# Optimization experiments

Measured on AMD Instinct MI355X. Metric: run time of the kernel, lower is better.

## Reference

```python
import jax, jax.numpy as jnp
import numpy as np

B, CIN, H, W = 16, 256, 48, 48
K, CD, MULTI = 64, 64, 1
GAMMA = (1.0 - 1e-10) ** (1.0 ** 0.6)  # iter = 1


def _ln(v, s, b, eps=1e-5):
    m = v.mean(-1, keepdims=True)
    var = ((v - m) ** 2).mean(-1, keepdims=True)
    return (v - m) / jnp.sqrt(var + eps) * s + b


def _spatial_masks():
    # pairwise squared distance between (i,j) grid coords, N = H*W
    ii, jj = jnp.meshgrid(jnp.arange(H, dtype=jnp.float32), jnp.arange(W, dtype=jnp.float32), indexing='ij')
    coord = jnp.stack([ii.ravel(), jj.ravel()], axis=1)  # [N,2]
    sq = (coord ** 2).sum(-1, keepdims=True)             # [N,1]
    d2 = sq - 2.0 * (coord @ coord.T) + sq.T             # [N,N]
    m = jnp.exp(-jnp.sqrt(jnp.abs(d2)))
    A = m / m.sum(0, keepdims=True)  # column-normalized (torch sums dim=1 of [B,N,N])
    cur, out = A, []
    for _ in range(MULTI):
        cur = cur @ A  # A^(num+2)
        out.append(cur)
    return out


def setup_inputs() -> dict:
    key = jax.random.key(0)
    ks = jax.random.split(key, 3)
    x = jax.random.normal(ks[0], (B, CIN, H, W), jnp.float32)
    clusters = jax.random.normal(ks[1], (1, K, CD), jnp.float32) * 0.1
    pi = jnp.ones((1, K), jnp.float32) / K
    cov = jnp.ones((1, K), jnp.float32)
    w_proj = jax.random.normal(ks[2], (CD, CIN), jnp.float32) / np.sqrt(CIN)
    nt_scale = jnp.ones((CD,), jnp.float32)
    nt_bias = jnp.zeros((CD,), jnp.float32)
    pn_scale = jnp.ones((K * MULTI,), jnp.float32)
    pn_bias = jnp.zeros((K * MULTI,), jnp.float32)
    return dict(x=x, clusters=clusters, pi=pi, cov=cov, w_proj=w_proj,
                nt_scale=nt_scale, nt_bias=nt_bias, pn_scale=pn_scale, pn_bias=pn_bias)


def reference(x, clusters, pi, cov, w_proj, nt_scale, nt_bias, pn_scale, pn_bias):
    N = H * W
    # 1x1 conv projection -> tokens [B,N,CD]
    xf = jnp.einsum('bihw,ci->bhwc', x, w_proj).reshape(B, N, CD)
    # normalized templates (batch-invariant)
    t = _ln(clusters[0], nt_scale, nt_bias)  # [K,CD]
    # squared euclidean distance via expansion (avoids [B,CD,N,K] intermediate)
    x2 = (xf ** 2).sum(-1)  # [B,N]
    t2 = (t ** 2).sum(-1)   # [K]
    d = x2[:, :, None] + t2[None, None, :] - 2.0 * jnp.einsum('bnc,kc->bnk', xf, t)
    logits = jnp.log(pi[0] / jnp.sqrt(cov[0])) - d / cov[0] / 2.0
    attn = jax.nn.softmax(logits, axis=-1)  # [B,N,K]
    # EM-style updates
    pi_new = pi + GAMMA * (attn.sum(1) / N - pi)                     # [B,K]
    attn_n = attn + 1e-8
    attn_n = attn_n / attn_n.sum(-2, keepdims=True)                  # normalize over N
    t_new = clusters + GAMMA * (jnp.einsum('bnc,bnk->bkc', xf, attn_n) - clusters)  # [B,K,CD]
    tn2 = (t_new ** 2).sum(-1)  # [B,K]
    d2 = x2[:, :, None] + tn2[:, None, :] - 2.0 * jnp.einsum('bnc,bkc->bnk', xf, t_new)
    cov_new = cov + GAMMA * ((d2 * attn_n).sum(1) - cov)             # [B,K]
    # spatial distance-encoding masks (stop-gradient / constant w.r.t. params)
    masks = _spatial_masks()
    outp = jnp.concatenate([jnp.einsum('bnk,nm->bkm', attn_n, M) for M in masks], axis=1)  # [B,K*MULTI,N]
    outp = _ln(outp.transpose(0, 2, 1), pn_scale, pn_bias).transpose(0, 2, 1)
    outp = outp.reshape(B, K * MULTI, H, W)
    attn_out = attn.transpose(0, 2, 1).reshape(B, K, H, W)
    return outp, attn_out, t_new, pi_new, cov_new
```

## Files before the change

### kernel.cpp

```cpp
#include <hip/hip_runtime.h>
#include <hip/hip_bf16.h>
#include <math.h>

#define B_   16
#define CIN_ 256
#define H_   48
#define W_   48
#define N_   2304
#define K_   64
#define CD_  64

#define GAMMA_F 0.9999999999f
#define LUT_N  4419

using f32x4  = __attribute__((ext_vector_type(4))) float;
using bf16x8 = __attribute__((ext_vector_type(8))) short;
using s16x4  = __attribute__((ext_vector_type(4))) short;

__device__ __forceinline__ void split_bf(float x, short& hi, short& lo) {
  unsigned u = __builtin_bit_cast(unsigned, x);
  unsigned r = (u + 0x7FFFu + ((u >> 16) & 1u)) & 0xFFFF0000u;
  hi = (short)(r >> 16);
  float res = x - __builtin_bit_cast(float, r);
  unsigned u2 = __builtin_bit_cast(unsigned, res);
  unsigned r2 = u2 + 0x7FFFu + ((u2 >> 16) & 1u);
  lo = (short)(r2 >> 16);
}

constexpr size_t OFF_XF    = 0;
constexpr size_t OFF_ANT   = OFF_XF    + (size_t)B_*N_*CD_;
constexpr size_t OFF_T     = OFF_ANT   + (size_t)B_*K_*N_;
constexpr size_t OFF_T2    = OFF_T     + (size_t)K_*CD_;
constexpr size_t OFF_LOGPI = OFF_T2    + K_;
constexpr size_t OFF_I2C   = OFF_LOGPI + K_;
constexpr size_t OFF_X2    = OFF_I2C   + K_;
constexpr size_t OFF_CS    = OFF_X2    + (size_t)B_*N_;
constexpr size_t OFF_ICN   = OFF_CS    + (size_t)B_*K_;
constexpr size_t OFF_MASKH = OFF_ICN   + (size_t)B_*K_;
constexpr size_t OFF_MASKL = OFF_MASKH + (size_t)N_*N_/2;

constexpr size_t OUT_OUTP = 0;
constexpr size_t OUT_ATTN = (size_t)B_*K_*N_;
constexpr size_t OUT_TNEW = OUT_ATTN + (size_t)B_*K_*N_;
constexpr size_t OUT_PI   = OUT_TNEW + (size_t)B_*K_*CD_;
constexpr size_t OUT_COV  = OUT_PI   + (size_t)B_*K_;

__global__ __launch_bounds__(256) void k_proj(const float* __restrict__ x, const float* __restrict__ wp,
                                              float* __restrict__ xf) {
  __shared__ float xs[32][64];
  __shared__ float ws_[32][65];
  int b = blockIdx.y, n0 = blockIdx.x * 64;
  int tid = threadIdx.x;
  int nn = tid & 63, cg = tid >> 6;
  float acc[16];
#pragma unroll
  for (int j = 0; j < 16; j++) acc[j] = 0.f;
  for (int i0 = 0; i0 < CIN_; i0 += 32) {
#pragma unroll
    for (int j = 0; j < 8; j++) {
      int ii = cg * 8 + j;
      xs[ii][nn] = x[((size_t)b * CIN_ + i0 + ii) * N_ + n0 + nn];
    }
    {
      int c = tid >> 2, iq = (tid & 3) * 8;
#pragma unroll
      for (int j = 0; j < 8; j++)
        ws_[iq + j][c] = wp[(size_t)c * CIN_ + i0 + iq + j];
    }
    __syncthreads();
#pragma unroll
    for (int ii = 0; ii < 32; ++ii) {
      float xv = xs[ii][nn];
#pragma unroll
      for (int j = 0; j < 16; j++) acc[j] += xv * ws_[ii][cg * 16 + j];
    }
    __syncthreads();
  }
  float* dst = xf + ((size_t)b * N_ + n0 + nn) * CD_ + cg * 16;
#pragma unroll
  for (int j4 = 0; j4 < 4; j4++)
    *(float4*)(dst + j4 * 4) = make_float4(acc[j4*4], acc[j4*4+1], acc[j4*4+2], acc[j4*4+3]);
}

__global__ void k_templ(const float* __restrict__ clusters, const float* __restrict__ pi,
                        const float* __restrict__ cov, const float* __restrict__ nsc,
                        const float* __restrict__ nbi, float* __restrict__ t, float* __restrict__ t2,
                        float* __restrict__ logpi, float* __restrict__ i2c) {
  int k = threadIdx.x;
  float v[CD_];
  float m = 0;
#pragma unroll
  for (int c = 0; c < CD_; c++) { v[c] = clusters[k * CD_ + c]; m += v[c]; }
  m /= CD_;
  float var = 0;
#pragma unroll
  for (int c = 0; c < CD_; c++) { float d = v[c] - m; var += d * d; }
  var /= CD_;
  float inv = 1.f / sqrtf(var + 1e-5f);
  float s2 = 0;
#pragma unroll
  for (int c = 0; c < CD_; c++) {
    float tv = (v[c] - m) * inv * nsc[c] + nbi[c];
    t[k * CD_ + c] = tv;
    s2 += tv * tv;
  }
  t2[k] = s2;
  float p = pi[k], cv = cov[k];
  logpi[k] = logf(p) - 0.5f * logf(cv);
  i2c[k] = 0.5f / cv;
}

__global__ __launch_bounds__(256) void k_attn(const float* __restrict__ xf, const float* __restrict__ t,
                                              const float* __restrict__ t2, const float* __restrict__ logpi,
                                              const float* __restrict__ i2c, float* __restrict__ ant,
                                              float* __restrict__ aout, float* __restrict__ x2o) {
  __shared__ __align__(16) float ts[K_ * CD_];
  __shared__ float t2s[K_], lps[K_], ics[K_];
  int tid = threadIdx.x;
  for (int i = tid; i < K_ * CD_; i += 256) ts[i] = t[i];
  if (tid < K_) { t2s[tid] = t2[tid]; lps[tid] = logpi[tid]; ics[tid] = i2c[tid]; }
  __syncthreads();
  int b = blockIdx.y;
  int n = blockIdx.x * 256 + tid;
  const float4* xr = (const float4*)(xf + ((size_t)b * N_ + n) * CD_);
  float4 xv[16];
#pragma unroll
  for (int i = 0; i < 16; i++) xv[i] = xr[i];
  float x2 = 0;
#pragma unroll
  for (int i = 0; i < 16; i++) x2 += xv[i].x * xv[i].x + xv[i].y * xv[i].y + xv[i].z * xv[i].z + xv[i].w * xv[i].w;
  x2o[(size_t)b * N_ + n] = x2;
  float lg[K_];
#pragma unroll
  for (int k = 0; k < K_; k++) {
    const float4* tk = (const float4*)(ts + k * CD_);
    float dot = 0;
#pragma unroll
    for (int i = 0; i < 16; i++) {
      float4 tv = tk[i];
      dot += xv[i].x * tv.x + xv[i].y * tv.y + xv[i].z * tv.z + xv[i].w * tv.w;
    }
    lg[k] = lps[k] - (x2 + t2s[k] - 2.f * dot) * ics[k];
  }
  float mx = lg[0];
#pragma unroll
  for (int k = 1; k < K_; k++) mx = fmaxf(mx, lg[k]);
  float sum = 0;
#pragma unroll
  for (int k = 0; k < K_; k++) { lg[k] = __expf(lg[k] - mx); sum += lg[k]; }
  float inv = 1.f / sum;
  size_t base = (size_t)b * K_ * N_ + n;
#pragma unroll
  for (int k = 0; k < K_; k++) {
    float v = lg[k] * inv;
    ant[base + (size_t)k * N_] = v;
    aout[base + (size_t)k * N_] = v;
  }
}

__global__ __launch_bounds__(256) void k_colsum2(const float* __restrict__ ant, float* __restrict__ colsum) {
  int r = blockIdx.x, tid = threadIdx.x;
  const float* row = ant + (size_t)r * N_;
  float s = 0;
  for (int n = tid; n < N_; n += 256) s += row[n];
#pragma unroll
  for (int off = 32; off; off >>= 1) s += __shfl_down(s, off);
  __shared__ float red[4];
  if ((tid & 63) == 0) red[tid >> 6] = s;
  __syncthreads();
  if (tid == 0) colsum[r] = red[0] + red[1] + red[2] + red[3];
}

__global__ void k_pinew(const float* __restrict__ colsum, const float* __restrict__ pi,
                        float* __restrict__ pi_out, float* __restrict__ icn) {
  int b = blockIdx.x, k = threadIdx.x;
  float cs = colsum[b * K_ + k];
  float p = pi[k];
  pi_out[b * K_ + k] = p + GAMMA_F * (cs / (float)N_ - p);
  icn[b * K_ + k] = 1.f / (cs + (float)N_ * 1e-8f);
}

__global__ __launch_bounds__(256) void k_tnew_cov(const float* __restrict__ ant, const float* __restrict__ icn,
                                                  const float* __restrict__ xf, const float* __restrict__ x2,
                                                  const float* __restrict__ clusters, const float* __restrict__ cov,
                                                  float* __restrict__ tnew_out, float* __restrict__ cov_out) {
  int k = blockIdx.x, b = blockIdx.y;
  int tid = threadIdx.x;
  int c = tid & 63, g = tid >> 6;
  const float* arow = ant + ((size_t)b * K_ + k) * N_;
  const float* x2r = x2 + (size_t)b * N_;
  float acc = 0, ax2 = 0;
#pragma unroll 4
  for (int n = g; n < N_; n += 4) {
    float a = arow[n] + 1e-8f;
    acc += a * xf[((size_t)b * N_ + n) * CD_ + c];
    ax2 += a * x2r[n];
  }
  __shared__ float red[4][64];
  __shared__ float red2[4];
  red[g][c] = acc;
  if (c == 0) red2[g] = ax2;
  __syncthreads();
  if (tid < 64) {
    float icnv = icn[b * K_ + k];
    float s = (red[0][c] + red[1][c] + red[2][c] + red[3][c]) * icnv;
    float cl = clusters[k * CD_ + c];
    float tv = cl + GAMMA_F * (s - cl);
    tnew_out[((size_t)b * K_ + k) * CD_ + c] = tv;
    float sq = tv * tv;
    float st = s * tv;
#pragma unroll
    for (int off = 32; off; off >>= 1) { sq += __shfl_down(sq, off); st += __shfl_down(st, off); }
    if (c == 0) {
      float ax2t = (red2[0] + red2[1] + red2[2] + red2[3]) * icnv;
      float cv = cov[k];
      float csum = ax2t + sq - 2.f * st;
      cov_out[b * K_ + k] = cv + GAMMA_F * (csum - cv);
    }
  }
}

__global__ __launch_bounds__(256) void k_amean(const float* __restrict__ ant, const float* __restrict__ icn,
                                               float* __restrict__ amean) {
  int b = blockIdx.y;
  int n = blockIdx.x * 256 + threadIdx.x;
  const float* base = ant + (size_t)b * K_ * N_ + n;
  const float* ic = icn + b * K_;
  float s = 0;
#pragma unroll 8
  for (int k = 0; k < K_; k++)
    s += (base[(size_t)k * N_] + 1e-8f) * ic[k];
  amean[(size_t)b * N_ + n] = s * (1.f / (float)K_);
}

__global__ __launch_bounds__(256) void k_mask(short* __restrict__ MH, short* __restrict__ ML) {
  __shared__ float lut[LUT_N];
  __shared__ float red[4];
  const int m = blockIdx.x;
  const int mi = m / W_, mj = m % W_;
  const int tid = threadIdx.x;
  for (int i = tid; i < LUT_N; i += 256) lut[i] = __expf(-sqrtf((float)i));
  __syncthreads();
  float e[N_ / 256];
  float s = 0;
#pragma unroll
  for (int it = 0; it < N_ / 256; it++) {
    int n = it * 256 + tid;
    int ni = n / W_, nj = n - (n / W_) * W_;
    int dx = ni - mi, dy = nj - mj;
    e[it] = lut[dx * dx + dy * dy];
    s += e[it];
  }
#pragma unroll
  for (int off = 32; off; off >>= 1) s += __shfl_down(s, off);
  if ((tid & 63) == 0) red[tid >> 6] = s;
  __syncthreads();
  const float imc = 1.f / (red[0] + red[1] + red[2] + red[3]);
#pragma unroll
  for (int it = 0; it < N_ / 256; it++) {
    int n = it * 256 + tid;
    short h, l;
    split_bf(e[it] * imc, h, l);
    MH[(size_t)m * N_ + n] = h;
    ML[(size_t)m * N_ + n] = l;
  }
}


__global__ __launch_bounds__(256) void gemm1_mfma(const float* __restrict__ Am, const float* __restrict__ icn,
                                                  const float* __restrict__ amean,
                                                  const short* __restrict__ MaskH, const short* __restrict__ MaskL,
                                                  short* __restrict__ YdH, short* __restrict__ YdL) {
  __shared__ __align__(16) short Ah[64][40];
  __shared__ __align__(16) short Al[64][40];
  __shared__ __align__(16) short Bh[64][40];
  __shared__ __align__(16) short Bl[64][40];
  const int tid = threadIdx.x;
  const int b = blockIdx.y;
  const int m0 = b * 64, n0 = blockIdx.x * 64;
  const int lane = tid & 63, w = tid >> 6;
  const int fr = lane & 15, quad = lane >> 4;
  const int srow = tid >> 2;
  const int skq  = (tid & 3) * 8;
  const float ic = icn[m0 + srow];
  const float badd = 1e-8f * ic;
  const size_t mrow = (size_t)(n0 + srow) * N_;
  f32x4 acc[4] = {};
  for (int k0 = 0; k0 < N_; k0 += 32) {
    const float* ap = Am + (size_t)(m0 + srow) * N_ + k0 + skq;
    const float* mp = amean + (size_t)b * N_ + k0 + skq;
    float va[8];
    {
      float4 a0 = *(const float4*)ap;
      float4 a1 = *(const float4*)(ap + 4);
      float4 u0 = *(const float4*)mp;
      float4 u1 = *(const float4*)(mp + 4);
      va[0] = fmaf(a0.x, ic, badd) - u0.x; va[1] = fmaf(a0.y, ic, badd) - u0.y;
      va[2] = fmaf(a0.z, ic, badd) - u0.z; va[3] = fmaf(a0.w, ic, badd) - u0.w;
      va[4] = fmaf(a1.x, ic, badd) - u1.x; va[5] = fmaf(a1.y, ic, badd) - u1.y;
      va[6] = fmaf(a1.z, ic, badd) - u1.z; va[7] = fmaf(a1.w, ic, badd) - u1.w;
    }
    bf16x8 avh, avl;
#pragma unroll
    for (int j = 0; j < 8; j++) { short h, l; split_bf(va[j], h, l); avh[j] = h; avl[j] = l; }
    *(bf16x8*)&Ah[srow][skq] = avh;
    *(bf16x8*)&Al[srow][skq] = avl;
    *(bf16x8*)&Bh[srow][skq] = *(const bf16x8*)&MaskH[mrow + k0 + skq];
    *(bf16x8*)&Bl[srow][skq] = *(const bf16x8*)&MaskL[mrow + k0 + skq];
    __syncthreads();
    bf16x8 afh = *(const bf16x8*)&Ah[w * 16 + fr][quad * 8];
    bf16x8 afl = *(const bf16x8*)&Al[w * 16 + fr][quad * 8];
#pragma unroll
    for (int ns = 0; ns < 4; ns++) {
      bf16x8 bfh = *(const bf16x8*)&Bh[ns * 16 + fr][quad * 8];
      bf16x8 bfl = *(const bf16x8*)&Bl[ns * 16 + fr][quad * 8];
      acc[ns] = __builtin_amdgcn_mfma_f32_16x16x32_bf16(afh, bfh, acc[ns], 0, 0, 0);
      acc[ns] = __builtin_amdgcn_mfma_f32_16x16x32_bf16(afh, bfl, acc[ns], 0, 0, 0);
      acc[ns] = __builtin_amdgcn_mfma_f32_16x16x32_bf16(afl, bfh, acc[ns], 0, 0, 0);
    }
    __syncthreads();
  }
  const size_t rbase = (size_t)(m0 + w * 16 + fr) * N_ + n0;
#pragma unroll
  for (int ns = 0; ns < 4; ns++) {
    s16x4 h4, l4;
#pragma unroll
    for (int reg = 0; reg < 4; reg++) { short h, l; split_bf(acc[ns][reg], h, l); h4[reg] = h; l4[reg] = l; }
    *(s16x4*)&YdH[rbase + ns * 16 + quad * 4] = h4;
    *(s16x4*)&YdL[rbase + ns * 16 + quad * 4] = l4;
  }
}

__global__ __launch_bounds__(256) void gemm2_ln_mfma(const short* __restrict__ YdH, const short* __restrict__ YdL,
                                                     const short* __restrict__ MaskH, const short* __restrict__ MaskL,
                                                     const float* __restrict__ pns, const float* __restrict__ pnb,
                                                     float* __restrict__ outp) {
  __shared__ __align__(16) short Ah[64][40];
  __shared__ __align__(16) short Al[64][40];
  __shared__ __align__(16) short Bh[64][40];
  __shared__ __align__(16) short Bl[64][40];
  __shared__ __align__(16) float S[64][68];
  __shared__ float rstd[64], sc[64], bi[64];
  const int tid = threadIdx.x;
  const int b = blockIdx.y;
  const int m0 = b * 64, n0 = blockIdx.x * 64;
  const int lane = tid & 63, w = tid >> 6;
  const int fr = lane & 15, quad = lane >> 4;
  const int srow = tid >> 2;
  const int skq  = (tid & 3) * 8;
  const size_t mrow = (size_t)(n0 + srow) * N_;
  if (tid < 64) { sc[tid] = pns[tid]; bi[tid] = pnb[tid]; }
  f32x4 acc[4] = {};
  for (int k0 = 0; k0 < N_; k0 += 32) {
    const size_t aoff = (size_t)(m0 + srow) * N_ + k0 + skq;
    *(bf16x8*)&Ah[srow][skq] = *(const bf16x8*)&YdH[aoff];
    *(bf16x8*)&Al[srow][skq] = *(const bf16x8*)&YdL[aoff];
    *(bf16x8*)&Bh[srow][skq] = *(const bf16x8*)&MaskH[mrow + k0 + skq];
    *(bf16x8*)&Bl[srow][skq] = *(const bf16x8*)&MaskL[mrow + k0 + skq];
    __syncthreads();
    bf16x8 afh = *(const bf16x8*)&Ah[w * 16 + fr][quad * 8];
    bf16x8 afl = *(const bf16x8*)&Al[w * 16 + fr][quad * 8];
#pragma unroll
    for (int ns = 0; ns < 4; ns++) {
      bf16x8 bfh = *(const bf16x8*)&Bh[ns * 16 + fr][quad * 8];
      bf16x8 bfl = *(const bf16x8*)&Bl[ns * 16 + fr][quad * 8];
      acc[ns] = __builtin_amdgcn_mfma_f32_16x16x32_bf16(afh, bfh, acc[ns], 0, 0, 0);
      acc[ns] = __builtin_amdgcn_mfma_f32_16x16x32_bf16(afh, bfl, acc[ns], 0, 0, 0);
      acc[ns] = __builtin_amdgcn_mfma_f32_16x16x32_bf16(afl, bfh, acc[ns], 0, 0, 0);
    }
    __syncthreads();
  }
#pragma unroll
  for (int ns = 0; ns < 4; ns++)
    *(f32x4*)&S[w * 16 + fr][ns * 16 + quad * 4] = acc[ns];
  __syncthreads();
  if (tid < 64) {
    float ss = 0;
#pragma unroll
    for (int k = 0; k < K_; k++) { float d = S[k][tid]; ss += d * d; }
    rstd[tid] = 1.f / sqrtf(ss / (float)K_ + 1e-5f);
  }
  __syncthreads();
  {
    int c = tid & 63, g = tid >> 6;
#pragma unroll
    for (int i = 0; i < 16; i++) {
      int r = g * 16 + i;
      outp[(size_t)(m0 + r) * N_ + n0 + c] = S[r][c] * rstd[c] * sc[r] + bi[r];
    }
  }
}

extern "C" void kernel_launch(void* const* d_in, const int* in_sizes, int n_in,
                              void* d_out, int out_size, void* d_ws, size_t ws_size,
                              hipStream_t stream) {
  const float* x        = (const float*)d_in[0];
  const float* clusters = (const float*)d_in[1];
  const float* pi       = (const float*)d_in[2];
  const float* cov      = (const float*)d_in[3];
  const float* w_proj   = (const float*)d_in[4];
  const float* nt_scale = (const float*)d_in[5];
  const float* nt_bias  = (const float*)d_in[6];
  const float* pn_scale = (const float*)d_in[7];
  const float* pn_bias  = (const float*)d_in[8];
  float* out = (float*)d_out;
  float* w = (float*)d_ws;
  short* YdH = (short*)(w + OFF_XF);
  short* YdL = YdH + (size_t)B_ * K_ * N_;
  short* MaskH = (short*)(w + OFF_MASKH);
  short* MaskL = (short*)(w + OFF_MASKL);

  k_mask<<<N_, 256, 0, stream>>>(MaskH, MaskL);
  k_proj<<<dim3(N_ / 64, B_), 256, 0, stream>>>(x, w_proj, w + OFF_XF);
  k_templ<<<1, K_, 0, stream>>>(clusters, pi, cov, nt_scale, nt_bias,
                                w + OFF_T, w + OFF_T2, w + OFF_LOGPI, w + OFF_I2C);
  k_attn<<<dim3(N_ / 256, B_), 256, 0, stream>>>(w + OFF_XF, w + OFF_T, w + OFF_T2,
                                                 w + OFF_LOGPI, w + OFF_I2C,
                                                 w + OFF_ANT, out + OUT_ATTN, w + OFF_X2);
  k_colsum2<<<B_ * K_, 256, 0, stream>>>(w + OFF_ANT, w + OFF_CS);
  k_pinew<<<B_, K_, 0, stream>>>(w + OFF_CS, pi, out + OUT_PI, w + OFF_ICN);
  k_tnew_cov<<<dim3(K_, B_), 256, 0, stream>>>(w + OFF_ANT, w + OFF_ICN, w + OFF_XF, w + OFF_X2,
                                               clusters, cov, out + OUT_TNEW, out + OUT_COV);
  k_amean<<<dim3(N_ / 256, B_), 256, 0, stream>>>(w + OFF_ANT, w + OFF_ICN, w + OFF_X2);
  gemm1_mfma<<<dim3(N_ / 64, B_), 256, 0, stream>>>(w + OFF_ANT, w + OFF_ICN, w + OFF_X2,
                                                    MaskH, MaskL, YdH, YdL);
  gemm2_ln_mfma<<<dim3(N_ / 64, B_), 256, 0, stream>>>(YdH, YdL, MaskH, MaskL,
                                                       pn_scale, pn_bias, out + OUT_OUTP);
}
```

Measured before the change: 415.6 us.

## Split attention softmax across 4 lanes per token, drop duplicate attn buffer and mask LUT

Measured after the change: 418.7 us. About the same (+0.7%).

```diff
diff --git a/kernel.cpp b/kernel.cpp
--- a/kernel.cpp
+++ b/kernel.cpp
@@ -11,7 +11,6 @@
 #define CD_  64
 
 #define GAMMA_F 0.9999999999f
-#define LUT_N  4419
 
 using f32x4  = __attribute__((ext_vector_type(4))) float;
 using bf16x8 = __attribute__((ext_vector_type(8))) short;
@@ -112,16 +111,17 @@
 
 __global__ __launch_bounds__(256) void k_attn(const float* __restrict__ xf, const float* __restrict__ t,
                                               const float* __restrict__ t2, const float* __restrict__ logpi,
-                                              const float* __restrict__ i2c, float* __restrict__ ant,
+                                              const float* __restrict__ i2c,
                                               float* __restrict__ aout, float* __restrict__ x2o) {
-  __shared__ __align__(16) float ts[K_ * CD_];
+  __shared__ __align__(16) float ts[K_][72];
   __shared__ float t2s[K_], lps[K_], ics[K_];
   int tid = threadIdx.x;
-  for (int i = tid; i < K_ * CD_; i += 256) ts[i] = t[i];
+  for (int i = tid; i < K_ * CD_; i += 256) ts[i >> 6][i & 63] = t[i];
   if (tid < K_) { t2s[tid] = t2[tid]; lps[tid] = logpi[tid]; ics[tid] = i2c[tid]; }
   __syncthreads();
   int b = blockIdx.y;
-  int n = blockIdx.x * 256 + tid;
+  int tok = tid >> 2, kg = tid & 3;
+  int n = blockIdx.x * 64 + tok;
   const float4* xr = (const float4*)(xf + ((size_t)b * N_ + n) * CD_);
   float4 xv[16];
 #pragma unroll
@@ -129,33 +129,35 @@
   float x2 = 0;
 #pragma unroll
   for (int i = 0; i < 16; i++) x2 += xv[i].x * xv[i].x + xv[i].y * xv[i].y + xv[i].z * xv[i].z + xv[i].w * xv[i].w;
-  x2o[(size_t)b * N_ + n] = x2;
-  float lg[K_];
-#pragma unroll
-  for (int k = 0; k < K_; k++) {
-    const float4* tk = (const float4*)(ts + k * CD_);
+  if (kg == 0) x2o[(size_t)b * N_ + n] = x2;
+  float lg[16];
+#pragma unroll
+  for (int kk = 0; kk < 16; kk++) {
+    int k = kk * 4 + kg;
+    const float4* tk = (const float4*)&ts[k][0];
     float dot = 0;
 #pragma unroll
     for (int i = 0; i < 16; i++) {
       float4 tv = tk[i];
       dot += xv[i].x * tv.x + xv[i].y * tv.y + xv[i].z * tv.z + xv[i].w * tv.w;
     }
-    lg[k] = lps[k] - (x2 + t2s[k] - 2.f * dot) * ics[k];
+    lg[kk] = lps[k] - (x2 + t2s[k] - 2.f * dot) * ics[k];
   }
   float mx = lg[0];
 #pragma unroll
-  for (int k = 1; k < K_; k++) mx = fmaxf(mx, lg[k]);
+  for (int kk = 1; kk < 16; kk++) mx = fmaxf(mx, lg[kk]);
+  mx = fmaxf(mx, __shfl_xor(mx, 1));
+  mx = fmaxf(mx, __shfl_xor(mx, 2));
   float sum = 0;
 #pragma unroll
-  for (int k = 0; k < K_; k++) { lg[k] = __expf(lg[k] - mx); sum += lg[k]; }
+  for (int kk = 0; kk < 16; kk++) { lg[kk] = __expf(lg[kk] - mx); sum += lg[kk]; }
+  sum += __shfl_xor(sum, 1);
+  sum += __shfl_xor(sum, 2);
   float inv = 1.f / sum;
   size_t base = (size_t)b * K_ * N_ + n;
 #pragma unroll
-  for (int k = 0; k < K_; k++) {
-    float v = lg[k] * inv;
-    ant[base + (size_t)k * N_] = v;
-    aout[base + (size_t)k * N_] = v;
-  }
+  for (int kk = 0; kk < 16; kk++)
+    aout[base + (size_t)(kk * 4 + kg) * N_] = lg[kk] * inv;
 }
 
 __global__ __launch_bounds__(256) void k_colsum2(const float* __restrict__ ant, float* __restrict__ colsum) {
@@ -234,13 +236,10 @@
 }
 
 __global__ __launch_bounds__(256) void k_mask(short* __restrict__ MH, short* __restrict__ ML) {
-  __shared__ float lut[LUT_N];
   __shared__ float red[4];
   const int m = blockIdx.x;
   const int mi = m / W_, mj = m % W_;
   const int tid = threadIdx.x;
-  for (int i = tid; i < LUT_N; i += 256) lut[i] = __expf(-sqrtf((float)i));
-  __syncthreads();
   float e[N_ / 256];
   float s = 0;
 #pragma unroll
@@ -248,7 +247,7 @@
     int n = it * 256 + tid;
     int ni = n / W_, nj = n - (n / W_) * W_;
     int dx = ni - mi, dy = nj - mj;
-    e[it] = lut[dx * dx + dy * dy];
+    e[it] = __expf(-sqrtf((float)(dx * dx + dy * dy)));
     s += e[it];
   }
 #pragma unroll
@@ -409,20 +408,21 @@
   short* YdL = YdH + (size_t)B_ * K_ * N_;
   short* MaskH = (short*)(w + OFF_MASKH);
   short* MaskL = (short*)(w + OFF_MASKL);
+  float* attn = out + OUT_ATTN;
 
   k_mask<<<N_, 256, 0, stream>>>(MaskH, MaskL);
   k_proj<<<dim3(N_ / 64, B_), 256, 0, stream>>>(x, w_proj, w + OFF_XF);
   k_templ<<<1, K_, 0, stream>>>(clusters, pi, cov, nt_scale, nt_bias,
                                 w + OFF_T, w + OFF_T2, w + OFF_LOGPI, w + OFF_I2C);
-  k_attn<<<dim3(N_ / 256, B_), 256, 0, stream>>>(w + OFF_XF, w + OFF_T, w + OFF_T2,
-                                                 w + OFF_LOGPI, w + OFF_I2C,
-                                                 w + OFF_ANT, out + OUT_ATTN, w + OFF_X2);
-  k_colsum2<<<B_ * K_, 256, 0, stream>>>(w + OFF_ANT, w + OFF_CS);
+  k_attn<<<dim3(N_ / 64, B_), 256, 0, stream>>>(w + OFF_XF, w + OFF_T, w + OFF_T2,
+                                                w + OFF_LOGPI, w + OFF_I2C,
+                                                attn, w + OFF_X2);
+  k_colsum2<<<B_ * K_, 256, 0, stream>>>(attn, w + OFF_CS);
   k_pinew<<<B_, K_, 0, stream>>>(w + OFF_CS, pi, out + OUT_PI, w + OFF_ICN);
-  k_tnew_cov<<<dim3(K_, B_), 256, 0, stream>>>(w + OFF_ANT, w + OFF_ICN, w + OFF_XF, w + OFF_X2,
+  k_tnew_cov<<<dim3(K_, B_), 256, 0, stream>>>(attn, w + OFF_ICN, w + OFF_XF, w + OFF_X2,
                                                clusters, cov, out + OUT_TNEW, out + OUT_COV);
-  k_amean<<<dim3(N_ / 256, B_), 256, 0, stream>>>(w + OFF_ANT, w + OFF_ICN, w + OFF_X2);
-  gemm1_mfma<<<dim3(N_ / 64, B_), 256, 0, stream>>>(w + OFF_ANT, w + OFF_ICN, w + OFF_X2,
+  k_amean<<<dim3(N_ / 256, B_), 256, 0, stream>>>(attn, w + OFF_ICN, w + OFF_X2);
+  gemm1_mfma<<<dim3(N_ / 64, B_), 256, 0, stream>>>(attn, w + OFF_ICN, w + OFF_X2,
                                                     MaskH, MaskL, YdH, YdL);
   gemm2_ln_mfma<<<dim3(N_ / 64, B_), 256, 0, stream>>>(YdH, YdL, MaskH, MaskL,
                                                        pn_scale, pn_bias, out + OUT_OUTP);
```
